# Optimization experiments

Measured on AMD Instinct MI355X. Metric: run time of the kernel, lower is better.

The kernel has to match this reference:

```python
import jax, jax.numpy as jnp
import numpy as np
import math

NUM_BUCKETS = 32
MAX_DISTANCE = 128
N_HEADS = 16
D_KV = 64


def _relative_position_bucket(relative_position, num_buckets=NUM_BUCKETS, max_distance=MAX_DISTANCE):
    # bidirectional (encoder) variant
    num_buckets //= 2
    relative_buckets = (relative_position > 0).astype(jnp.int32) * num_buckets
    rp = jnp.abs(relative_position)
    max_exact = num_buckets // 2
    is_small = rp < max_exact
    rp_large = max_exact + (
        jnp.log(jnp.maximum(rp, 1).astype(jnp.float32) / max_exact)
        / math.log(max_distance / max_exact)
        * (num_buckets - max_exact)
    ).astype(jnp.int32)
    rp_large = jnp.minimum(rp_large, num_buckets - 1)
    return relative_buckets + jnp.where(is_small, rp, rp_large)


def compute_bias(rel_bias, q_len, k_len):
    ctx = jnp.arange(q_len)[:, None]
    mem = jnp.arange(k_len)[None, :]
    buckets = _relative_position_bucket(mem - ctx)          # [q, k]
    values = rel_bias[buckets]                               # [q, k, h]
    return jnp.transpose(values, (2, 0, 1))[None]            # [1, h, q, k]


def setup_inputs() -> dict:
    key = jax.random.key(0)
    ks = jax.random.split(key, 6)
    d_model, inner = 1024, N_HEADS * D_KV
    s = 0.02
    return {
        "hidden_states": jax.random.normal(ks[0], (2, 2048, d_model), jnp.float32),
        "Wq": jax.random.normal(ks[1], (d_model, inner), jnp.float32) * s,
        "Wk": jax.random.normal(ks[2], (d_model, inner), jnp.float32) * s,
        "Wv": jax.random.normal(ks[3], (d_model, inner), jnp.float32) * s,
        "Wo": jax.random.normal(ks[4], (inner, d_model), jnp.float32) * s,
        "rel_bias": jax.random.normal(ks[5], (NUM_BUCKETS, N_HEADS), jnp.float32) * s,
    }


def reference(hidden_states, Wq, Wk, Wv, Wo, rel_bias):
    B, S, D = hidden_states.shape

    def split_heads(x):  # [B,S,inner] -> [B,H,S,dk]
        return x.reshape(B, S, N_HEADS, D_KV).transpose(0, 2, 1, 3)

    q = split_heads(hidden_states @ Wq)
    k = split_heads(hidden_states @ Wk)
    v = split_heads(hidden_states @ Wv)

    # T5 does NOT scale by 1/sqrt(d_kv)
    scores = jnp.einsum("bhqd,bhkd->bhqk", q, k)
    scores = scores + compute_bias(rel_bias, S, S)
    attn = jax.nn.softmax(scores, axis=-1)
    ctx = jnp.einsum("bhqk,bhkd->bhqd", attn, v)
    ctx = ctx.transpose(0, 2, 1, 3).reshape(B, S, N_HEADS * D_KV)
    return ctx @ Wo
```

## Files before the change

### kernel.cpp

```cpp
#include <hip/hip_runtime.h>
#include <hip/hip_bf16.h>

typedef __bf16 bf16x8 __attribute__((ext_vector_type(8)));
typedef __bf16 bf16x4 __attribute__((ext_vector_type(4)));
typedef float floatx4 __attribute__((ext_vector_type(4)));
using bf16 = __hip_bfloat16;

#define S_    2048
#define NHEAD 16
#define LOG2E 1.4426950408889634f

__device__ __forceinline__ void load_lds16(const bf16* g, void* lds) {
  __builtin_amdgcn_global_load_lds((const __attribute__((address_space(1))) void*)g,
                                   (__attribute__((address_space(3))) void*)lds, 16, 0, 0);
}

__global__ void cast_f32_bf16_kernel(const float* __restrict__ src, bf16* __restrict__ dst) {
  int i = (blockIdx.x * 256 + threadIdx.x) * 4;
  float4 v = *(const float4*)(src + i);
  bf16 o[4] = {__float2bfloat16(v.x), __float2bfloat16(v.y),
               __float2bfloat16(v.z), __float2bfloat16(v.w)};
  *(uint2*)(dst + i) = *(const uint2*)o;
}

__global__ void transpose_w_kernel(const float* __restrict__ wq, const float* __restrict__ wk,
                                   const float* __restrict__ wv, const float* __restrict__ wo,
                                   bf16* __restrict__ wt_qkv, bf16* __restrict__ wt_o) {
  __shared__ bf16 tile[32][33];
  int mat = blockIdx.z;
  const float* src = (mat == 0) ? wq : (mat == 1) ? wk : (mat == 2) ? wv : wo;
  bf16* dst = (mat == 3) ? wt_o : wt_qkv + mat * 1024 * 1024;
  int tx = threadIdx.x, ty = threadIdx.y;
  int n0 = blockIdx.x * 32, k0 = blockIdx.y * 32;
#pragma unroll
  for (int j = 0; j < 32; j += 8)
    tile[ty + j][tx] = __float2bfloat16(src[(k0 + ty + j) * 1024 + n0 + tx]);
  __syncthreads();
#pragma unroll
  for (int j = 0; j < 32; j += 8)
    dst[(n0 + ty + j) * 1024 + k0 + tx] = tile[tx][ty + j];
}

__global__ void bias_table_kernel(const float* __restrict__ rel_bias, float* __restrict__ tab) {
  int idx = blockIdx.x * 256 + threadIdx.x;
  int h = idx >> 12, j = idx & 4095;
  int delta = j - 2048;
  int rb = (delta > 0) ? 16 : 0;
  int rpa = delta < 0 ? -delta : delta;
  int bsmall;
  if (rpa < 8) {
    bsmall = rpa;
  } else {
    int lg = 25 - __clz(rpa * rpa);
    bsmall = 8 + lg;
    if (bsmall > 15) bsmall = 15;
  }
  tab[idx] = rel_bias[(rb + bsmall) * 16 + h] * LOG2E;
}

__global__ __launch_bounds__(256) void gemm_qkv_kernel(const bf16* __restrict__ A,
                                                       const bf16* __restrict__ Bt,
                                                       bf16* __restrict__ qh,
                                                       bf16* __restrict__ kf,
                                                       bf16* __restrict__ vf) {
  const int K = 1024;
  __shared__ bf16 As[128 * 32];
  __shared__ bf16 Bs[128 * 32];
  int t = threadIdx.x;
  int m0 = blockIdx.y * 128, n0 = blockIdx.x * 128;
  int w = t >> 6, lane = t & 63, ln = lane & 15, quad = lane >> 4;
  int wr = w >> 1, wc = w & 1;
  floatx4 acc[4][4];
  floatx4 zero = {0.f, 0.f, 0.f, 0.f};
#pragma unroll
  for (int i = 0; i < 4; i++)
#pragma unroll
    for (int j = 0; j < 4; j++) acc[i][j] = zero;

  int r = t >> 2, c = (t & 3) * 8;
  const bf16* Ag = A + (long)(m0 + r) * K + c;
  const bf16* Bg = Bt + (long)(n0 + r) * K + c;
  char* ldsA0 = (char*)As + w * 1024;
  char* ldsA1 = ldsA0 + 4096;
  char* ldsB0 = (char*)Bs + w * 1024;
  char* ldsB1 = ldsB0 + 4096;

  for (int k0 = 0; k0 < K; k0 += 32) {
    load_lds16(Ag + k0, ldsA0);
    load_lds16(Ag + (long)64 * K + k0, ldsA1);
    load_lds16(Bg + k0, ldsB0);
    load_lds16(Bg + (long)64 * K + k0, ldsB1);
    __syncthreads();
    bf16x8 af[4], bfv[4];
#pragma unroll
    for (int i = 0; i < 4; i++)
      af[i] = *(const bf16x8*)&As[(wr * 64 + i * 16 + ln) * 32 + quad * 8];
#pragma unroll
    for (int j = 0; j < 4; j++)
      bfv[j] = *(const bf16x8*)&Bs[(wc * 64 + j * 16 + ln) * 32 + quad * 8];
#pragma unroll
    for (int i = 0; i < 4; i++)
#pragma unroll
      for (int j = 0; j < 4; j++)
        acc[i][j] = __builtin_amdgcn_mfma_f32_16x16x32_bf16(af[i], bfv[j], acc[i][j], 0, 0, 0);
    __syncthreads();
  }

  int nb = n0 + wc * 64;
  int type = nb >> 10, h = (nb >> 6) & 15;
  int b = (m0 >> 11);
  int sl0 = (m0 & 2047) + wr * 64;
  long bhbase = (long)((b * 16 + h)) * 131072;

  if (type == 0) {
#pragma unroll
    for (int i = 0; i < 4; i++)
#pragma unroll
      for (int j = 0; j < 4; j++) {
        int d = j * 16 + ln;
#pragma unroll
        for (int rr = 0; rr < 4; rr++) {
          int s = sl0 + i * 16 + quad * 4 + rr;
          qh[bhbase + (long)s * 64 + d] = __float2bfloat16(acc[i][j][rr]);
        }
      }
  } else if (type == 1) {
#pragma unroll
    for (int i = 0; i < 4; i++)
#pragma unroll
      for (int j = 0; j < 4; j++) {
        int d = j * 16 + ln;
        int dpart = (d >> 5) * 512 + ((d >> 3) & 3) * 128 + (d & 7);
        int kb = (sl0 + i * 16) * 64;
#pragma unroll
        for (int rr = 0; rr < 4; rr++)
          kf[bhbase + kb + dpart + (quad * 4 + rr) * 8] = __float2bfloat16(acc[i][j][rr]);
      }
  } else {
#pragma unroll
    for (int i = 0; i < 4; i++)
#pragma unroll
      for (int j = 0; j < 4; j++) {
        int off = (sl0 + (i >> 1) * 32) * 64 + j * 512 +
                  ((quad >> 1) + ((i & 1) << 1)) * 128 + ln * 8 + (quad & 1) * 4;
        bf16x4 pk = {(__bf16)acc[i][j][0], (__bf16)acc[i][j][1],
                     (__bf16)acc[i][j][2], (__bf16)acc[i][j][3]};
        *(bf16x4*)(vf + bhbase + off) = pk;
      }
  }
}

__global__ __launch_bounds__(256, 2) void attn_kernel(const bf16* __restrict__ qh,
                                                      const bf16* __restrict__ kf,
                                                      const bf16* __restrict__ vf,
                                                      const float* __restrict__ btab,
                                                      bf16* __restrict__ ctx) {
  __shared__ char PsRaw[4 * 4096];
  __shared__ char Ks[2][8192];
  int t = threadIdx.x, w = t >> 6, lane = t & 63, ln = lane & 15, quad = lane >> 4;
  int bh = blockIdx.x, b = bh >> 4, h = bh & 15;
  int qw = blockIdx.y * 128 + w * 32;

  const bf16* qbase = qh + (long)bh * S_ * 64;
  const bf16* kfb = kf + (long)bh * S_ * 64;
  const bf16* vfb = vf + (long)bh * S_ * 64;
  const float* bt = btab + h * 4096;
  char* myPs = PsRaw + w * 4096;
  int lbo = quad * 256 + ln * 16;
  int foff = quad * 128 + ln * 8;

  bf16x8 Qf[2][2];
#pragma unroll
  for (int g = 0; g < 2; g++) {
    const bf16* qr = qbase + (long)(qw + g * 16 + ln) * 64;
    Qf[g][0] = *(const bf16x8*)(qr + quad * 8);
    Qf[g][1] = *(const bf16x8*)(qr + 32 + quad * 8);
  }

  float cneg = bt[0], cpos = bt[4095];
  float l_acc[2] = {0.f, 0.f};
  floatx4 o[2][4];
  floatx4 zero = {0.f, 0.f, 0.f, 0.f};
#pragma unroll
  for (int g = 0; g < 2; g++)
#pragma unroll
    for (int dt = 0; dt < 4; dt++) o[g][dt] = zero;

  load_lds16(kfb + t * 8, Ks[0] + w * 1024);
  load_lds16(kfb + 2048 + t * 8, Ks[0] + 4096 + w * 1024);
  bf16x8 Vc[4][2], Vn[4][2];
#pragma unroll
  for (int f = 0; f < 2; f++)
#pragma unroll
    for (int dt = 0; dt < 4; dt++)
      Vc[dt][f] = *(const bf16x8*)(vfb + f * 2048 + dt * 512 + foff);

  int pb = 0;
  for (int k0 = 0; k0 < S_; k0 += 64) {
    __syncthreads();
    int kn = k0 + 64;
    if (kn < S_) {
      const bf16* kg = kfb + (long)kn * 64 + t * 8;
      load_lds16(kg, Ks[pb ^ 1] + w * 1024);
      load_lds16(kg + 2048, Ks[pb ^ 1] + 4096 + w * 1024);
      const bf16* vp = vfb + (long)kn * 64;
#pragma unroll
      for (int f = 0; f < 2; f++)
#pragma unroll
        for (int dt = 0; dt < 4; dt++)
          Vn[dt][f] = *(const bf16x8*)(vp + f * 2048 + dt * 512 + foff);
    }

    const char* bK = Ks[pb];
    bf16x8 Kr[4][2];
#pragma unroll
    for (int tile = 0; tile < 4; tile++) {
      Kr[tile][0] = *(const bf16x8*)(bK + tile * 2048 + lbo);
      Kr[tile][1] = *(const bf16x8*)(bK + tile * 2048 + 1024 + lbo);
    }

    bool near = (k0 > qw - 192) && (k0 < qw + 160);
#pragma unroll
    for (int g = 0; g < 2; g++) {
      char* ps = myPs + g * 2048;
      floatx4 st[4];
#pragma unroll
      for (int tile = 0; tile < 4; tile++) {
        st[tile] = __builtin_amdgcn_mfma_f32_16x16x32_bf16(Kr[tile][0], Qf[g][0], zero, 0, 0, 0);
        st[tile] = __builtin_amdgcn_mfma_f32_16x16x32_bf16(Kr[tile][1], Qf[g][1], st[tile], 0, 0, 0);
      }
      if (near) {
#pragma unroll
        for (int tile = 0; tile < 4; tile++) {
          int bidx = k0 + tile * 16 + quad * 4 - (qw + g * 16 + ln) + 2048;
          float p0 = __builtin_amdgcn_exp2f(fmaf(st[tile][0], LOG2E, bt[bidx + 0]));
          float p1 = __builtin_amdgcn_exp2f(fmaf(st[tile][1], LOG2E, bt[bidx + 1]));
          float p2 = __builtin_amdgcn_exp2f(fmaf(st[tile][2], LOG2E, bt[bidx + 2]));
          float p3 = __builtin_amdgcn_exp2f(fmaf(st[tile][3], LOG2E, bt[bidx + 3]));
          l_acc[g] += (p0 + p1) + (p2 + p3);
          bf16x4 pk = {(__bf16)p0, (__bf16)p1, (__bf16)p2, (__bf16)p3};
          int chunk = tile * 2 + (quad >> 1);
          *(bf16x4*)(ps + (ln * 8 + (chunk ^ (ln & 7))) * 16 + (quad & 1) * 8) = pk;
        }
      } else {
        float cb = (k0 > qw) ? cpos : cneg;
#pragma unroll
        for (int tile = 0; tile < 4; tile++) {
          float p0 = __builtin_amdgcn_exp2f(fmaf(st[tile][0], LOG2E, cb));
          float p1 = __builtin_amdgcn_exp2f(fmaf(st[tile][1], LOG2E, cb));
          float p2 = __builtin_amdgcn_exp2f(fmaf(st[tile][2], LOG2E, cb));
          float p3 = __builtin_amdgcn_exp2f(fmaf(st[tile][3], LOG2E, cb));
          l_acc[g] += (p0 + p1) + (p2 + p3);
          bf16x4 pk = {(__bf16)p0, (__bf16)p1, (__bf16)p2, (__bf16)p3};
          int chunk = tile * 2 + (quad >> 1);
          *(bf16x4*)(ps + (ln * 8 + (chunk ^ (ln & 7))) * 16 + (quad & 1) * 8) = pk;
        }
      }
    }

#pragma unroll
    for (int g = 0; g < 2; g++) {
      char* ps = myPs + g * 2048;
      bf16x8 Pf0 = *(const bf16x8*)(ps + (ln * 8 + (quad ^ (ln & 7))) * 16);
      bf16x8 Pf1 = *(const bf16x8*)(ps + (ln * 8 + ((4 + quad) ^ (ln & 7))) * 16);
#pragma unroll
      for (int dt = 0; dt < 4; dt++) {
        o[g][dt] = __builtin_amdgcn_mfma_f32_16x16x32_bf16(Pf0, Vc[dt][0], o[g][dt], 0, 0, 0);
        o[g][dt] = __builtin_amdgcn_mfma_f32_16x16x32_bf16(Pf1, Vc[dt][1], o[g][dt], 0, 0, 0);
      }
    }

    if (kn < S_) {
#pragma unroll
      for (int dt = 0; dt < 4; dt++) {
        Vc[dt][0] = Vn[dt][0]; Vc[dt][1] = Vn[dt][1];
      }
    }
    pb ^= 1;
  }

#pragma unroll
  for (int g = 0; g < 2; g++) {
    l_acc[g] += __shfl_xor(l_acc[g], 16);
    l_acc[g] += __shfl_xor(l_acc[g], 32);
  }
#pragma unroll
  for (int g = 0; g < 2; g++)
#pragma unroll
    for (int rr = 0; rr < 4; rr++) {
      float linv = 1.0f / __shfl(l_acc[g], quad * 4 + rr);
      int q = qw + g * 16 + quad * 4 + rr;
#pragma unroll
      for (int dt = 0; dt < 4; dt++)
        ctx[(long)(b * S_ + q) * 1024 + h * 64 + dt * 16 + ln] =
            __float2bfloat16(o[g][dt][rr] * linv);
    }
}

__global__ __launch_bounds__(256) void gemm_bt_kernel(const bf16* __restrict__ A,
                                                      const bf16* __restrict__ Bt,
                                                      float* __restrict__ C,
                                                      int M, int N, int K) {
  __shared__ bf16 As[128 * 32];
  __shared__ bf16 Bs[128 * 32];
  int t = threadIdx.x;
  int m0 = blockIdx.y * 128, n0 = blockIdx.x * 128;
  int w = t >> 6, lane = t & 63, ln = lane & 15, quad = lane >> 4;
  int wr = w >> 1, wc = w & 1;
  floatx4 acc[4][4];
  floatx4 zero = {0.f, 0.f, 0.f, 0.f};
#pragma unroll
  for (int i = 0; i < 4; i++)
#pragma unroll
    for (int j = 0; j < 4; j++) acc[i][j] = zero;

  int r = t >> 2, c = (t & 3) * 8;
  const bf16* Ag = A + (long)(m0 + r) * K + c;
  const bf16* Bg = Bt + (long)(n0 + r) * K + c;
  char* ldsA0 = (char*)As + w * 1024;
  char* ldsA1 = ldsA0 + 4096;
  char* ldsB0 = (char*)Bs + w * 1024;
  char* ldsB1 = ldsB0 + 4096;

  for (int k0 = 0; k0 < K; k0 += 32) {
    load_lds16(Ag + k0, ldsA0);
    load_lds16(Ag + (long)64 * K + k0, ldsA1);
    load_lds16(Bg + k0, ldsB0);
    load_lds16(Bg + (long)64 * K + k0, ldsB1);
    __syncthreads();
    bf16x8 af[4], bfv[4];
#pragma unroll
    for (int i = 0; i < 4; i++)
      af[i] = *(const bf16x8*)&As[(wr * 64 + i * 16 + ln) * 32 + quad * 8];
#pragma unroll
    for (int j = 0; j < 4; j++)
      bfv[j] = *(const bf16x8*)&Bs[(wc * 64 + j * 16 + ln) * 32 + quad * 8];
#pragma unroll
    for (int i = 0; i < 4; i++)
#pragma unroll
      for (int j = 0; j < 4; j++)
        acc[i][j] = __builtin_amdgcn_mfma_f32_16x16x32_bf16(af[i], bfv[j], acc[i][j], 0, 0, 0);
    __syncthreads();
  }

#pragma unroll
  for (int i = 0; i < 4; i++)
#pragma unroll
    for (int j = 0; j < 4; j++)
#pragma unroll
      for (int rr = 0; rr < 4; rr++)
        C[(long)(m0 + wr * 64 + i * 16 + quad * 4 + rr) * N + n0 + wc * 64 + j * 16 + ln] =
            acc[i][j][rr];
}

extern "C" void kernel_launch(void* const* d_in, const int* in_sizes, int n_in,
                              void* d_out, int out_size, void* d_ws, size_t ws_size,
                              hipStream_t stream) {
  (void)in_sizes; (void)n_in; (void)out_size; (void)ws_size;
  const float* hidden   = (const float*)d_in[0];
  const float* Wq       = (const float*)d_in[1];
  const float* Wk       = (const float*)d_in[2];
  const float* Wv       = (const float*)d_in[3];
  const float* Wo       = (const float*)d_in[4];
  const float* rel_bias = (const float*)d_in[5];

  char* ws = (char*)d_ws;
  bf16*  hbf    = (bf16*)(ws + 0);
  bf16*  wt_qkv = (bf16*)(ws + 8388608);
  bf16*  wt_o   = (bf16*)(ws + 14680064);
  float* btab   = (float*)(ws + 16777216);
  bf16*  qh     = (bf16*)(ws + 17039360);
  bf16*  kf     = (bf16*)(ws + 25427968);
  bf16*  vf     = (bf16*)(ws + 33816576);
  bf16*  ctx    = (bf16*)(ws + 42205184);

  cast_f32_bf16_kernel<<<dim3(4096), dim3(256), 0, stream>>>(hidden, hbf);
  transpose_w_kernel<<<dim3(32, 32, 4), dim3(32, 8), 0, stream>>>(Wq, Wk, Wv, Wo, wt_qkv, wt_o);
  bias_table_kernel<<<dim3(256), dim3(256), 0, stream>>>(rel_bias, btab);
  gemm_qkv_kernel<<<dim3(24, 32), dim3(256), 0, stream>>>(hbf, wt_qkv, qh, kf, vf);
  attn_kernel<<<dim3(32, 16), dim3(256), 0, stream>>>(qh, kf, vf, btab, ctx);
  gemm_bt_kernel<<<dim3(8, 32), dim3(256), 0, stream>>>(ctx, wt_o, (float*)d_out, 4096, 1024, 1024);
}
```

Measured before the change: 206.6 us.

## Split attention over key halves, stage V via LDS, fuse prep kernels

Attention gains a second grid dimension that splits the key range in two, doubling the block count from 512 to 1024 so more CUs are busy. Each split writes unnormalised fp32 partial outputs and row sums, and a new reduce kernel combines them and normalises. V tiles are now loaded asynchronously into LDS next to K instead of through registers, and the P buffer is halved by handling one query group at a time. The three preprocessing kernels are merged into one launch. The cost is extra fp32 partial traffic (about 32 MB written and read) plus one more kernel launch.

After: 206.4 us. About the same (-0.1%).

```diff
diff --git a/kernel.cpp b/kernel.cpp
--- a/kernel.cpp
+++ b/kernel.cpp
@@ -15,47 +15,52 @@
                                    (__attribute__((address_space(3))) void*)lds, 16, 0, 0);
 }
 
-__global__ void cast_f32_bf16_kernel(const float* __restrict__ src, bf16* __restrict__ dst) {
-  int i = (blockIdx.x * 256 + threadIdx.x) * 4;
-  float4 v = *(const float4*)(src + i);
-  bf16 o[4] = {__float2bfloat16(v.x), __float2bfloat16(v.y),
-               __float2bfloat16(v.z), __float2bfloat16(v.w)};
-  *(uint2*)(dst + i) = *(const uint2*)o;
-}
-
-__global__ void transpose_w_kernel(const float* __restrict__ wq, const float* __restrict__ wk,
-                                   const float* __restrict__ wv, const float* __restrict__ wo,
-                                   bf16* __restrict__ wt_qkv, bf16* __restrict__ wt_o) {
+__global__ void prep_kernel(const float* __restrict__ hidden,
+                            const float* __restrict__ wq, const float* __restrict__ wk,
+                            const float* __restrict__ wv, const float* __restrict__ wo,
+                            const float* __restrict__ rel_bias,
+                            bf16* __restrict__ hbf, bf16* __restrict__ wt_qkv,
+                            bf16* __restrict__ wt_o, float* __restrict__ btab) {
   __shared__ bf16 tile[32][33];
-  int mat = blockIdx.z;
-  const float* src = (mat == 0) ? wq : (mat == 1) ? wk : (mat == 2) ? wv : wo;
-  bf16* dst = (mat == 3) ? wt_o : wt_qkv + mat * 1024 * 1024;
-  int tx = threadIdx.x, ty = threadIdx.y;
-  int n0 = blockIdx.x * 32, k0 = blockIdx.y * 32;
-#pragma unroll
-  for (int j = 0; j < 32; j += 8)
-    tile[ty + j][tx] = __float2bfloat16(src[(k0 + ty + j) * 1024 + n0 + tx]);
-  __syncthreads();
-#pragma unroll
-  for (int j = 0; j < 32; j += 8)
-    dst[(n0 + ty + j) * 1024 + k0 + tx] = tile[tx][ty + j];
-}
-
-__global__ void bias_table_kernel(const float* __restrict__ rel_bias, float* __restrict__ tab) {
-  int idx = blockIdx.x * 256 + threadIdx.x;
-  int h = idx >> 12, j = idx & 4095;
-  int delta = j - 2048;
-  int rb = (delta > 0) ? 16 : 0;
-  int rpa = delta < 0 ? -delta : delta;
-  int bsmall;
-  if (rpa < 8) {
-    bsmall = rpa;
+  int bx = blockIdx.x, t = threadIdx.x;
+  if (bx < 2048) {
+    int i = (bx * 256 + t) * 8;
+    float4 v0 = *(const float4*)(hidden + i);
+    float4 v1 = *(const float4*)(hidden + i + 4);
+    bf16 o8[8] = {__float2bfloat16(v0.x), __float2bfloat16(v0.y),
+                  __float2bfloat16(v0.z), __float2bfloat16(v0.w),
+                  __float2bfloat16(v1.x), __float2bfloat16(v1.y),
+                  __float2bfloat16(v1.z), __float2bfloat16(v1.w)};
+    *(uint4*)(hbf + i) = *(const uint4*)o8;
+  } else if (bx < 6144) {
+    int mat = (bx - 2048) >> 10, tb = (bx - 2048) & 1023;
+    int n0 = (tb & 31) * 32, k0 = (tb >> 5) * 32;
+    const float* src = (mat == 0) ? wq : (mat == 1) ? wk : (mat == 2) ? wv : wo;
+    bf16* dst = (mat == 3) ? wt_o : wt_qkv + mat * 1024 * 1024;
+    int tx = t & 31, ty = t >> 5;
+#pragma unroll
+    for (int j = 0; j < 32; j += 8)
+      tile[ty + j][tx] = __float2bfloat16(src[(k0 + ty + j) * 1024 + n0 + tx]);
+    __syncthreads();
+#pragma unroll
+    for (int j = 0; j < 32; j += 8)
+      dst[(n0 + ty + j) * 1024 + k0 + tx] = tile[tx][ty + j];
   } else {
-    int lg = 25 - __clz(rpa * rpa);
-    bsmall = 8 + lg;
-    if (bsmall > 15) bsmall = 15;
-  }
-  tab[idx] = rel_bias[(rb + bsmall) * 16 + h] * LOG2E;
+    int idx = (bx - 6144) * 256 + t;
+    int h = idx >> 12, j = idx & 4095;
+    int delta = j - 2048;
+    int rb = (delta > 0) ? 16 : 0;
+    int rpa = delta < 0 ? -delta : delta;
+    int bsmall;
+    if (rpa < 8) {
+      bsmall = rpa;
+    } else {
+      int lg = 25 - __clz(rpa * rpa);
+      bsmall = 8 + lg;
+      if (bsmall > 15) bsmall = 15;
+    }
+    btab[idx] = rel_bias[(rb + bsmall) * 16 + h] * LOG2E;
+  }
 }
 
 __global__ __launch_bounds__(256) void gemm_qkv_kernel(const bf16* __restrict__ A,
@@ -154,20 +159,21 @@
                                                       const bf16* __restrict__ kf,
                                                       const bf16* __restrict__ vf,
                                                       const float* __restrict__ btab,
-                                                      bf16* __restrict__ ctx) {
-  __shared__ char PsRaw[4 * 4096];
-  __shared__ char Ks[2][8192];
+                                                      float* __restrict__ opart,
+                                                      float* __restrict__ lpart) {
+  __shared__ char KV[2][16384];
+  __shared__ char PsRaw[4 * 2048];
   int t = threadIdx.x, w = t >> 6, lane = t & 63, ln = lane & 15, quad = lane >> 4;
-  int bh = blockIdx.x, b = bh >> 4, h = bh & 15;
+  int bh = blockIdx.x, h = bh & 15;
   int qw = blockIdx.y * 128 + w * 32;
+  int ks = blockIdx.z, kbase0 = ks * 1024;
 
   const bf16* qbase = qh + (long)bh * S_ * 64;
-  const bf16* kfb = kf + (long)bh * S_ * 64;
-  const bf16* vfb = vf + (long)bh * S_ * 64;
+  const bf16* kfb = kf + (long)bh * S_ * 64 + (long)kbase0 * 64;
+  const bf16* vfb = vf + (long)bh * S_ * 64 + (long)kbase0 * 64;
   const float* bt = btab + h * 4096;
-  char* myPs = PsRaw + w * 4096;
+  char* myPs = PsRaw + w * 2048;
   int lbo = quad * 256 + ln * 16;
-  int foff = quad * 128 + ln * 8;
 
   bf16x8 Qf[2][2];
 #pragma unroll
@@ -186,43 +192,42 @@
 #pragma unroll
     for (int dt = 0; dt < 4; dt++) o[g][dt] = zero;
 
-  load_lds16(kfb + t * 8, Ks[0] + w * 1024);
-  load_lds16(kfb + 2048 + t * 8, Ks[0] + 4096 + w * 1024);
-  bf16x8 Vc[4][2], Vn[4][2];
-#pragma unroll
-  for (int f = 0; f < 2; f++)
-#pragma unroll
-    for (int dt = 0; dt < 4; dt++)
-      Vc[dt][f] = *(const bf16x8*)(vfb + f * 2048 + dt * 512 + foff);
+  load_lds16(kfb + t * 8, KV[0] + w * 1024);
+  load_lds16(kfb + 2048 + t * 8, KV[0] + 4096 + w * 1024);
+  load_lds16(vfb + t * 8, KV[0] + 8192 + w * 1024);
+  load_lds16(vfb + 2048 + t * 8, KV[0] + 12288 + w * 1024);
 
   int pb = 0;
-  for (int k0 = 0; k0 < S_; k0 += 64) {
-    __syncthreads();
-    int kn = k0 + 64;
-    if (kn < S_) {
-      const bf16* kg = kfb + (long)kn * 64 + t * 8;
-      load_lds16(kg, Ks[pb ^ 1] + w * 1024);
-      load_lds16(kg + 2048, Ks[pb ^ 1] + 4096 + w * 1024);
-      const bf16* vp = vfb + (long)kn * 64;
-#pragma unroll
-      for (int f = 0; f < 2; f++)
-#pragma unroll
-        for (int dt = 0; dt < 4; dt++)
-          Vn[dt][f] = *(const bf16x8*)(vp + f * 2048 + dt * 512 + foff);
-    }
-
-    const char* bK = Ks[pb];
-    bf16x8 Kr[4][2];
+  for (int it = 0; it < 16; it++) {
+    int k0 = kbase0 + it * 64;
+    __syncthreads();
+    if (it < 15) {
+      const bf16* kg = kfb + (it + 1) * 4096 + t * 8;
+      const bf16* vg = vfb + (it + 1) * 4096 + t * 8;
+      char* nb_ = KV[pb ^ 1];
+      load_lds16(kg, nb_ + w * 1024);
+      load_lds16(kg + 2048, nb_ + 4096 + w * 1024);
+      load_lds16(vg, nb_ + 8192 + w * 1024);
+      load_lds16(vg + 2048, nb_ + 12288 + w * 1024);
+    }
+
+    const char* bK = KV[pb];
+    const char* bV = KV[pb] + 8192;
+    bf16x8 Kr[4][2], Vr[4][2];
 #pragma unroll
     for (int tile = 0; tile < 4; tile++) {
       Kr[tile][0] = *(const bf16x8*)(bK + tile * 2048 + lbo);
       Kr[tile][1] = *(const bf16x8*)(bK + tile * 2048 + 1024 + lbo);
     }
+#pragma unroll
+    for (int f = 0; f < 2; f++)
+#pragma unroll
+      for (int dt = 0; dt < 4; dt++)
+        Vr[dt][f] = *(const bf16x8*)(bV + f * 4096 + dt * 1024 + lbo);
 
     bool near = (k0 > qw - 192) && (k0 < qw + 160);
 #pragma unroll
     for (int g = 0; g < 2; g++) {
-      char* ps = myPs + g * 2048;
       floatx4 st[4];
 #pragma unroll
       for (int tile = 0; tile < 4; tile++) {
@@ -240,7 +245,7 @@
           l_acc[g] += (p0 + p1) + (p2 + p3);
           bf16x4 pk = {(__bf16)p0, (__bf16)p1, (__bf16)p2, (__bf16)p3};
           int chunk = tile * 2 + (quad >> 1);
-          *(bf16x4*)(ps + (ln * 8 + (chunk ^ (ln & 7))) * 16 + (quad & 1) * 8) = pk;
+          *(bf16x4*)(myPs + (ln * 8 + (chunk ^ (ln & 7))) * 16 + (quad & 1) * 8) = pk;
         }
       } else {
         float cb = (k0 > qw) ? cpos : cneg;
@@ -253,48 +258,52 @@
           l_acc[g] += (p0 + p1) + (p2 + p3);
           bf16x4 pk = {(__bf16)p0, (__bf16)p1, (__bf16)p2, (__bf16)p3};
           int chunk = tile * 2 + (quad >> 1);
-          *(bf16x4*)(ps + (ln * 8 + (chunk ^ (ln & 7))) * 16 + (quad & 1) * 8) = pk;
+          *(bf16x4*)(myPs + (ln * 8 + (chunk ^ (ln & 7))) * 16 + (quad & 1) * 8) = pk;
         }
       }
-    }
-
-#pragma unroll
-    for (int g = 0; g < 2; g++) {
-      char* ps = myPs + g * 2048;
-      bf16x8 Pf0 = *(const bf16x8*)(ps + (ln * 8 + (quad ^ (ln & 7))) * 16);
-      bf16x8 Pf1 = *(const bf16x8*)(ps + (ln * 8 + ((4 + quad) ^ (ln & 7))) * 16);
+
+      bf16x8 Pf0 = *(const bf16x8*)(myPs + (ln * 8 + (quad ^ (ln & 7))) * 16);
+      bf16x8 Pf1 = *(const bf16x8*)(myPs + (ln * 8 + ((4 + quad) ^ (ln & 7))) * 16);
 #pragma unroll
       for (int dt = 0; dt < 4; dt++) {
-        o[g][dt] = __builtin_amdgcn_mfma_f32_16x16x32_bf16(Pf0, Vc[dt][0], o[g][dt], 0, 0, 0);
-        o[g][dt] = __builtin_amdgcn_mfma_f32_16x16x32_bf16(Pf1, Vc[dt][1], o[g][dt], 0, 0, 0);
-      }
-    }
-
-    if (kn < S_) {
-#pragma unroll
-      for (int dt = 0; dt < 4; dt++) {
-        Vc[dt][0] = Vn[dt][0]; Vc[dt][1] = Vn[dt][1];
+        o[g][dt] = __builtin_amdgcn_mfma_f32_16x16x32_bf16(Pf0, Vr[dt][0], o[g][dt], 0, 0, 0);
+        o[g][dt] = __builtin_amdgcn_mfma_f32_16x16x32_bf16(Pf1, Vr[dt][1], o[g][dt], 0, 0, 0);
       }
     }
     pb ^= 1;
   }
 
+  long obase = ((long)(ks * 32 + bh)) * S_ * 64;
 #pragma unroll
   for (int g = 0; g < 2; g++) {
     l_acc[g] += __shfl_xor(l_acc[g], 16);
     l_acc[g] += __shfl_xor(l_acc[g], 32);
-  }
-#pragma unroll
-  for (int g = 0; g < 2; g++)
+    if (quad == 0)
+      lpart[(long)(ks * 32 + bh) * S_ + qw + g * 16 + ln] = l_acc[g];
 #pragma unroll
     for (int rr = 0; rr < 4; rr++) {
-      float linv = 1.0f / __shfl(l_acc[g], quad * 4 + rr);
       int q = qw + g * 16 + quad * 4 + rr;
 #pragma unroll
       for (int dt = 0; dt < 4; dt++)
-        ctx[(long)(b * S_ + q) * 1024 + h * 64 + dt * 16 + ln] =
-            __float2bfloat16(o[g][dt][rr] * linv);
-    }
+        opart[obase + (long)q * 64 + dt * 16 + ln] = o[g][dt][rr];
+    }
+  }
+}
+
+__global__ void reduce_kernel(const float* __restrict__ opart,
+                              const float* __restrict__ lpart,
+                              bf16* __restrict__ ctx) {
+  long flat = ((long)blockIdx.x * 256 + threadIdx.x) * 4;
+  int d = flat & 63;
+  int q = (int)((flat >> 6) & 2047);
+  int bh = (int)(flat >> 17);
+  long base = ((long)bh * S_ + q) * 64 + d;
+  float4 o0 = *(const float4*)(opart + base);
+  float4 o1 = *(const float4*)(opart + 4194304 + base);
+  float inv = 1.0f / (lpart[(long)bh * S_ + q] + lpart[65536 + (long)bh * S_ + q]);
+  bf16x4 pk = {(__bf16)((o0.x + o1.x) * inv), (__bf16)((o0.y + o1.y) * inv),
+               (__bf16)((o0.z + o1.z) * inv), (__bf16)((o0.w + o1.w) * inv)};
+  *(bf16x4*)(ctx + ((long)((bh >> 4) * S_ + q)) * 1024 + (bh & 15) * 64 + d) = pk;
 }
 
 __global__ __launch_bounds__(256) void gemm_bt_kernel(const bf16* __restrict__ A,
@@ -373,11 +382,13 @@
   bf16*  kf     = (bf16*)(ws + 25427968);
   bf16*  vf     = (bf16*)(ws + 33816576);
   bf16*  ctx    = (bf16*)(ws + 42205184);
-
-  cast_f32_bf16_kernel<<<dim3(4096), dim3(256), 0, stream>>>(hidden, hbf);
-  transpose_w_kernel<<<dim3(32, 32, 4), dim3(32, 8), 0, stream>>>(Wq, Wk, Wv, Wo, wt_qkv, wt_o);
-  bias_table_kernel<<<dim3(256), dim3(256), 0, stream>>>(rel_bias, btab);
+  float* opart  = (float*)(ws + 50593792);
+  float* lpart  = (float*)(ws + 84148224);
+
+  prep_kernel<<<dim3(6400), dim3(256), 0, stream>>>(hidden, Wq, Wk, Wv, Wo, rel_bias,
+                                                    hbf, wt_qkv, wt_o, btab);
   gemm_qkv_kernel<<<dim3(24, 32), dim3(256), 0, stream>>>(hbf, wt_qkv, qh, kf, vf);
-  attn_kernel<<<dim3(32, 16), dim3(256), 0, stream>>>(qh, kf, vf, btab, ctx);
+  attn_kernel<<<dim3(32, 16, 2), dim3(256), 0, stream>>>(qh, kf, vf, btab, opart, lpart);
+  reduce_kernel<<<dim3(4096), dim3(256), 0, stream>>>(opart, lpart, ctx);
   gemm_bt_kernel<<<dim3(8, 32), dim3(256), 0, stream>>>(ctx, wt_o, (float*)d_out, 4096, 1024, 1024);
 }
```
